# Optimization experiments

Hardware: AMD Instinct MI355X
Metric: run time of the kernel (lower is better)

## Reference

```python
import jax, jax.numpy as jnp
import numpy as np

N = 1_048_576   # number of input points
C = 64          # feature channels
GRID = 128      # voxels per spatial dim
BATCH = 4


def setup_inputs() -> dict:
    key = jax.random.key(0)
    k1, k2, k3 = jax.random.split(key, 3)
    # coords layout per scn: [x, y, z, batch_idx]
    xyz = jax.random.randint(k1, (N, 3), 0, GRID, dtype=jnp.int64)
    b = jax.random.randint(k2, (N, 1), 0, BATCH, dtype=jnp.int64)
    coords = jnp.concatenate([xyz, b], axis=1)
    features = jax.random.normal(k3, (N, C), dtype=jnp.float32)
    spatial_size = jnp.array([GRID, GRID, GRID], dtype=jnp.int64)
    return {"coords": coords, "features": features,
            "spatial_size": spatial_size, "batch_size": BATCH}


def reference(coords, features, spatial_size, batch_size):
    # Hash each (batch, x, y, z) coordinate to a unique linear voxel id,
    # then scatter-SUM (scn mode=3) features of duplicate coordinates.
    n = coords.shape[0]
    # row-major strides over spatial dims: [S1*S2, S2, 1]
    strides = jnp.concatenate([
        jnp.cumprod(spatial_size[::-1])[::-1][1:], jnp.ones((1,), jnp.int64)])
    vol = jnp.prod(spatial_size)
    lin = coords[:, -1] * vol + coords[:, :-1] @ strides  # [N] voxel ids

    # Unique active sites (padded to fixed size N for jit) + inverse map.
    uniq_ids, inv = jnp.unique(lin, size=n, fill_value=-1, return_inverse=True)
    inv = inv.reshape(n)

    # Scatter-reduce features into active sites (mode 3 = sum duplicates).
    sparse_features = jax.ops.segment_sum(features, inv, num_segments=n)
    return uniq_ids, sparse_features
```

## Files before the change

kernel.cpp:

```cpp
#include <hip/hip_runtime.h>

constexpr int GRID_D = 128;
constexpr int BATCHN = 4;
constexpr int C = 64;
constexpr int VOL = GRID_D * GRID_D * GRID_D;
constexpr int V = BATCHN * VOL;
constexpr int W = V / 32;
constexpr int SCAN_BS = 1024;
constexpr int SCAN_NB = W / SCAN_BS;


__global__ void zero_ws(uint4* __restrict__ p) {
    int i = blockIdx.x * blockDim.x + threadIdx.x;
    p[i] = uint4{0u, 0u, 0u, 0u};
}

__global__ void fill_neg1(float* out, int n) {
    int i = blockIdx.x * blockDim.x + threadIdx.x;
    if (i < n) out[i] = -1.0f;
}

__global__ void mark_bits(const int* __restrict__ coords, unsigned* __restrict__ bm,
                          unsigned* __restrict__ dup, int n) {
    int i = blockIdx.x * blockDim.x + threadIdx.x;
    if (i >= n) return;
    int4 co = reinterpret_cast<const int4*>(coords)[i];
    int lin = co.w * VOL + co.x * (GRID_D * GRID_D) + co.y * GRID_D + co.z;
    unsigned bit = 1u << (lin & 31);
    unsigned old = atomicOr(&bm[lin >> 5], bit);
    if (old & bit) atomicOr(&dup[lin >> 5], bit);
}

__global__ void scan1(const unsigned* __restrict__ bm, unsigned* __restrict__ wp,
                      unsigned* __restrict__ bs) {
    int idx = blockIdx.x * SCAN_BS + threadIdx.x;
    unsigned pc = __popc(bm[idx]);
    unsigned v = pc;
    #pragma unroll
    for (int d = 1; d < 64; d <<= 1) {
        unsigned t = __shfl_up(v, d, 64);
        if ((threadIdx.x & 63) >= d) v += t;
    }
    __shared__ unsigned wsum[16];
    int wid = threadIdx.x >> 6;
    int lane = threadIdx.x & 63;
    if (lane == 63) wsum[wid] = v;
    __syncthreads();
    if (threadIdx.x < 16) {
        unsigned s = wsum[threadIdx.x];
        #pragma unroll
        for (int d = 1; d < 16; d <<= 1) {
            unsigned t = __shfl_up(s, d, 16);
            if ((threadIdx.x & 15) >= d) s += t;
        }
        wsum[threadIdx.x] = s;
    }
    __syncthreads();
    unsigned waveoff = (wid == 0) ? 0u : wsum[wid - 1];
    wp[idx] = waveoff + v - pc;
    if (threadIdx.x == SCAN_BS - 1) bs[blockIdx.x] = waveoff + v;
}

__global__ void scan2(unsigned* bs, unsigned* total) {
    int t = threadIdx.x;
    unsigned pc = bs[t];
    unsigned v = pc;
    #pragma unroll
    for (int d = 1; d < 64; d <<= 1) {
        unsigned tt = __shfl_up(v, d, 64);
        if ((t & 63) >= d) v += tt;
    }
    __shared__ unsigned wsum[4];
    int wid = t >> 6, lane = t & 63;
    if (lane == 63) wsum[wid] = v;
    __syncthreads();
    if (t < 4) {
        unsigned s = wsum[t];
        #pragma unroll
        for (int d = 1; d < 4; d <<= 1) {
            unsigned tt = __shfl_up(s, d, 4);
            if ((t & 3) >= d) s += tt;
        }
        wsum[t] = s;
    }
    __syncthreads();
    unsigned waveoff = (wid == 0) ? 0u : wsum[wid - 1];
    bs[t] = waveoff + v - pc;
    if (t == SCAN_NB - 1) *total = waveoff + v;
}

__global__ void add_offsets(unsigned* __restrict__ wp, const unsigned* __restrict__ bs) {
    int idx = blockIdx.x * blockDim.x + threadIdx.x;
    wp[idx] += bs[idx >> 10];
}

__global__ void emit_uniq(const unsigned* __restrict__ bm, const unsigned* __restrict__ wp,
                          float* __restrict__ out) {
    int idx = blockIdx.x * blockDim.x + threadIdx.x;
    unsigned word = bm[idx];
    unsigned base = wp[idx];
    while (word) {
        int b = __ffs(word) - 1;
        out[base++] = (float)((idx << 5) + b);
        word &= word - 1;
    }
}

__global__ void zero_dup(const unsigned* __restrict__ bm, const unsigned* __restrict__ dup,
                         const unsigned* __restrict__ wp, float* __restrict__ outf) {
    int idx = blockIdx.x * blockDim.x + threadIdx.x;
    unsigned d = dup[idx];
    if (!d) return;
    unsigned word = bm[idx];
    unsigned base = wp[idx];
    while (d) {
        int b = __ffs(d) - 1;
        unsigned rank = base + __popc(word & ((1u << b) - 1u));
        float4* p = reinterpret_cast<float4*>(outf + (size_t)rank * C);
        #pragma unroll
        for (int i = 0; i < 16; i++) p[i] = float4{0.f, 0.f, 0.f, 0.f};
        d &= d - 1;
    }
}

__global__ void zero_tail(float* __restrict__ outf, const unsigned* __restrict__ total, int n) {
    int gid = blockIdx.x * blockDim.x + threadIdx.x;
    int rank = gid >> 4;
    if (rank >= n || rank < (int)*total) return;
    reinterpret_cast<float4*>(outf)[gid] = float4{0.f, 0.f, 0.f, 0.f};
}

__global__ void scatter_feat(const int* __restrict__ coords, const float4* __restrict__ feat4,
                             const unsigned* __restrict__ bm, const unsigned* __restrict__ dup,
                             const unsigned* __restrict__ wp, float* __restrict__ outf, int n) {
    int gid = blockIdx.x * blockDim.x + threadIdx.x;
    int pt = gid >> 4;
    int c4 = gid & 15;
    if (pt >= n) return;
    int4 co = reinterpret_cast<const int4*>(coords)[pt];
    int lin = co.w * VOL + co.x * (GRID_D * GRID_D) + co.y * GRID_D + co.z;
    int w = lin >> 5, b = lin & 31;
    unsigned rank = wp[w] + __popc(bm[w] & ((1u << b) - 1u));
    float4 v = feat4[(size_t)pt * 16 + c4];
    float* dst = outf + (size_t)rank * C + c4 * 4;
    if (dup[w] & (1u << b)) {
        atomicAdd(dst + 0, v.x);
        atomicAdd(dst + 1, v.y);
        atomicAdd(dst + 2, v.z);
        atomicAdd(dst + 3, v.w);
    } else {
        *reinterpret_cast<float4*>(dst) = v;
    }
}


extern "C" void kernel_launch(void* const* d_in, const int* in_sizes, int n_in,
                              void* d_out, int out_size, void* d_ws, size_t ws_size,
                              hipStream_t stream) {
    const int* coords = (const int*)d_in[0];
    const float* feat = (const float*)d_in[1];
    int n = in_sizes[0] / 4;

    float* out_ids = (float*)d_out;
    float* out_feat = (float*)d_out + n;

    unsigned* bm = (unsigned*)d_ws;
    unsigned* dup = bm + W;
    unsigned* wp = dup + W;
    unsigned* bs = wp + W;
    unsigned* total = bs + SCAN_NB;

    zero_ws<<<(2 * W * 4 / 16) / 256, 256, 0, stream>>>((uint4*)bm);

    fill_neg1<<<(n + 255) / 256, 256, 0, stream>>>(out_ids, n);
    mark_bits<<<(n + 255) / 256, 256, 0, stream>>>(coords, bm, dup, n);
    scan1<<<SCAN_NB, SCAN_BS, 0, stream>>>(bm, wp, bs);
    scan2<<<1, SCAN_NB, 0, stream>>>(bs, total);
    add_offsets<<<W / 1024, 1024, 0, stream>>>(wp, bs);
    emit_uniq<<<W / 256, 256, 0, stream>>>(bm, wp, out_ids);
    zero_dup<<<W / 256, 256, 0, stream>>>(bm, dup, wp, out_feat);
    zero_tail<<<(n * 16 + 255) / 256, 256, 0, stream>>>(out_feat, total, n);

    int scatter_threads = n * 16;
    scatter_feat<<<(scatter_threads + 255) / 256, 256, 0, stream>>>(
        coords, (const float4*)feat, bm, dup, wp, out_feat, n);
}
```

Before: 242.4 us.

## Fuse scan offset add and tail fills, cache linear ids, use nontemporal feature I/O

Drops the add_offsets pass by adding the block prefix at each consumer, and merges fill_neg1 into the tail zeroing kernel. The scan total now lives in bs[SCAN_NB]. mark_bits stores each point's linear voxel id so scatter reads 4 bytes per point instead of the 16-byte coord. Feature loads and non-duplicate stores use nontemporal builtins to avoid polluting cache. The changes cut kernel launches and passes over memory, at the cost of an extra 4 MB id buffer write and read.

```diff
diff --git a/kernel.cpp b/kernel.cpp
--- a/kernel.cpp
+++ b/kernel.cpp
@@ -9,26 +9,25 @@
 constexpr int SCAN_BS = 1024;
 constexpr int SCAN_NB = W / SCAN_BS;
 
+typedef float floatx4 __attribute__((ext_vector_type(4)));
+
 
 __global__ void zero_ws(uint4* __restrict__ p) {
     int i = blockIdx.x * blockDim.x + threadIdx.x;
     p[i] = uint4{0u, 0u, 0u, 0u};
 }
 
-__global__ void fill_neg1(float* out, int n) {
-    int i = blockIdx.x * blockDim.x + threadIdx.x;
-    if (i < n) out[i] = -1.0f;
-}
-
 __global__ void mark_bits(const int* __restrict__ coords, unsigned* __restrict__ bm,
-                          unsigned* __restrict__ dup, int n) {
+                          unsigned* __restrict__ dup, unsigned* __restrict__ lin,
+                          int n) {
     int i = blockIdx.x * blockDim.x + threadIdx.x;
     if (i >= n) return;
     int4 co = reinterpret_cast<const int4*>(coords)[i];
-    int lin = co.w * VOL + co.x * (GRID_D * GRID_D) + co.y * GRID_D + co.z;
-    unsigned bit = 1u << (lin & 31);
-    unsigned old = atomicOr(&bm[lin >> 5], bit);
-    if (old & bit) atomicOr(&dup[lin >> 5], bit);
+    unsigned l = (unsigned)(co.w * VOL + co.x * (GRID_D * GRID_D) + co.y * GRID_D + co.z);
+    lin[i] = l;
+    unsigned bit = 1u << (l & 31);
+    unsigned old = atomicOr(&bm[l >> 5], bit);
+    if (old & bit) atomicOr(&dup[l >> 5], bit);
 }
 
 __global__ void scan1(const unsigned* __restrict__ bm, unsigned* __restrict__ wp,
@@ -61,7 +60,7 @@
     if (threadIdx.x == SCAN_BS - 1) bs[blockIdx.x] = waveoff + v;
 }
 
-__global__ void scan2(unsigned* bs, unsigned* total) {
+__global__ void scan2(unsigned* bs) {
     int t = threadIdx.x;
     unsigned pc = bs[t];
     unsigned v = pc;
@@ -86,19 +85,14 @@
     __syncthreads();
     unsigned waveoff = (wid == 0) ? 0u : wsum[wid - 1];
     bs[t] = waveoff + v - pc;
-    if (t == SCAN_NB - 1) *total = waveoff + v;
-}
-
-__global__ void add_offsets(unsigned* __restrict__ wp, const unsigned* __restrict__ bs) {
-    int idx = blockIdx.x * blockDim.x + threadIdx.x;
-    wp[idx] += bs[idx >> 10];
+    if (t == SCAN_NB - 1) bs[SCAN_NB] = waveoff + v;
 }
 
 __global__ void emit_uniq(const unsigned* __restrict__ bm, const unsigned* __restrict__ wp,
-                          float* __restrict__ out) {
+                          const unsigned* __restrict__ bs, float* __restrict__ out) {
     int idx = blockIdx.x * blockDim.x + threadIdx.x;
     unsigned word = bm[idx];
-    unsigned base = wp[idx];
+    unsigned base = wp[idx] + bs[idx >> 10];
     while (word) {
         int b = __ffs(word) - 1;
         out[base++] = (float)((idx << 5) + b);
@@ -106,13 +100,24 @@
     }
 }
 
+__global__ void tail_fill(float* __restrict__ out_ids, float* __restrict__ outf,
+                          const unsigned* __restrict__ bs, int n) {
+    int gid = blockIdx.x * blockDim.x + threadIdx.x;
+    int rank = gid >> 4;
+    unsigned total = bs[SCAN_NB];
+    if (rank >= n || rank < (int)total) return;
+    reinterpret_cast<float4*>(outf)[gid] = float4{0.f, 0.f, 0.f, 0.f};
+    if ((gid & 15) == 0) out_ids[rank] = -1.0f;
+}
+
 __global__ void zero_dup(const unsigned* __restrict__ bm, const unsigned* __restrict__ dup,
-                         const unsigned* __restrict__ wp, float* __restrict__ outf) {
+                         const unsigned* __restrict__ wp, const unsigned* __restrict__ bs,
+                         float* __restrict__ outf) {
     int idx = blockIdx.x * blockDim.x + threadIdx.x;
     unsigned d = dup[idx];
     if (!d) return;
     unsigned word = bm[idx];
-    unsigned base = wp[idx];
+    unsigned base = wp[idx] + bs[idx >> 10];
     while (d) {
         int b = __ffs(d) - 1;
         unsigned rank = base + __popc(word & ((1u << b) - 1u));
@@ -123,25 +128,18 @@
     }
 }
 
-__global__ void zero_tail(float* __restrict__ outf, const unsigned* __restrict__ total, int n) {
-    int gid = blockIdx.x * blockDim.x + threadIdx.x;
-    int rank = gid >> 4;
-    if (rank >= n || rank < (int)*total) return;
-    reinterpret_cast<float4*>(outf)[gid] = float4{0.f, 0.f, 0.f, 0.f};
-}
-
-__global__ void scatter_feat(const int* __restrict__ coords, const float4* __restrict__ feat4,
+__global__ void scatter_feat(const unsigned* __restrict__ lin, const floatx4* __restrict__ feat4,
                              const unsigned* __restrict__ bm, const unsigned* __restrict__ dup,
-                             const unsigned* __restrict__ wp, float* __restrict__ outf, int n) {
+                             const unsigned* __restrict__ wp, const unsigned* __restrict__ bs,
+                             float* __restrict__ outf, int n) {
     int gid = blockIdx.x * blockDim.x + threadIdx.x;
     int pt = gid >> 4;
     int c4 = gid & 15;
     if (pt >= n) return;
-    int4 co = reinterpret_cast<const int4*>(coords)[pt];
-    int lin = co.w * VOL + co.x * (GRID_D * GRID_D) + co.y * GRID_D + co.z;
-    int w = lin >> 5, b = lin & 31;
-    unsigned rank = wp[w] + __popc(bm[w] & ((1u << b) - 1u));
-    float4 v = feat4[(size_t)pt * 16 + c4];
+    unsigned l = lin[pt];
+    unsigned w = l >> 5, b = l & 31;
+    unsigned rank = wp[w] + bs[w >> 10] + __popc(bm[w] & ((1u << b) - 1u));
+    floatx4 v = __builtin_nontemporal_load(&feat4[(size_t)pt * 16 + c4]);
     float* dst = outf + (size_t)rank * C + c4 * 4;
     if (dup[w] & (1u << b)) {
         atomicAdd(dst + 0, v.x);
@@ -149,7 +147,7 @@
         atomicAdd(dst + 2, v.z);
         atomicAdd(dst + 3, v.w);
     } else {
-        *reinterpret_cast<float4*>(dst) = v;
+        __builtin_nontemporal_store(v, reinterpret_cast<floatx4*>(dst));
     }
 }
 
@@ -168,20 +166,18 @@
     unsigned* dup = bm + W;
     unsigned* wp = dup + W;
     unsigned* bs = wp + W;
-    unsigned* total = bs + SCAN_NB;
+    unsigned* lin = bs + SCAN_NB + 63;
 
-    zero_ws<<<(2 * W * 4 / 16) / 256, 256, 0, stream>>>((uint4*)bm);
+    zero_ws<<<(2 * W) / (4 * 256), 256, 0, stream>>>((uint4*)bm);
 
-    fill_neg1<<<(n + 255) / 256, 256, 0, stream>>>(out_ids, n);
-    mark_bits<<<(n + 255) / 256, 256, 0, stream>>>(coords, bm, dup, n);
+    mark_bits<<<(n + 255) / 256, 256, 0, stream>>>(coords, bm, dup, lin, n);
     scan1<<<SCAN_NB, SCAN_BS, 0, stream>>>(bm, wp, bs);
-    scan2<<<1, SCAN_NB, 0, stream>>>(bs, total);
-    add_offsets<<<W / 1024, 1024, 0, stream>>>(wp, bs);
-    emit_uniq<<<W / 256, 256, 0, stream>>>(bm, wp, out_ids);
-    zero_dup<<<W / 256, 256, 0, stream>>>(bm, dup, wp, out_feat);
-    zero_tail<<<(n * 16 + 255) / 256, 256, 0, stream>>>(out_feat, total, n);
+    scan2<<<1, SCAN_NB, 0, stream>>>(bs);
+    emit_uniq<<<W / 256, 256, 0, stream>>>(bm, wp, bs, out_ids);
+    tail_fill<<<(n * 16 + 255) / 256, 256, 0, stream>>>(out_ids, out_feat, bs, n);
+    zero_dup<<<W / 256, 256, 0, stream>>>(bm, dup, wp, bs, out_feat);
 
     int scatter_threads = n * 16;
     scatter_feat<<<(scatter_threads + 255) / 256, 256, 0, stream>>>(
-        coords, (const float4*)feat, bm, dup, wp, out_feat, n);
+        lin, (const floatx4*)feat, bm, dup, wp, bs, out_feat, n);
 }
```

After: 227.2 us. 6.3% less time.
